# Performance work log

Hardware: AMD Instinct MI355X
Metric: run time of the kernel (lower is better)

Reference implementation:

```python
import jax, jax.numpy as jnp
import numpy as np

B, N, E, H = 4, 2048, 1024, 16
D = E // H  # head dim = 64


def setup_inputs() -> dict:
    key = jax.random.key(0)
    k1, k2, k3 = jax.random.split(key, 3)
    x = jax.random.normal(k1, (B, N, E), dtype=jnp.float32)
    # torch nn.Linear weights are [out_features, in_features]
    w_qkv = jax.random.normal(k2, (3 * E, E), dtype=jnp.float32) * (E ** -0.5)
    w_out = jax.random.normal(k3, (E, E), dtype=jnp.float32) * (E ** -0.5)
    return {"x": x, "w_qkv": w_qkv, "w_out": w_out}


def reference(x, w_qkv, w_out):
    # fused QKV projection: [B,N,E] @ [E,3E] -> [B,N,3E]
    qkv = jnp.einsum("bne,fe->bnf", x, w_qkv)
    q, k, v = jnp.split(qkv, 3, axis=-1)
    # b n (h d) -> b h n d
    split_heads = lambda t: t.reshape(B, N, H, D).transpose(0, 2, 1, 3)
    q, k, v = map(split_heads, (q, k, v))
    scale = D ** -0.5
    scores = jnp.einsum("bhnd,bhmd->bhnm", q, k) * scale
    attn = jax.nn.softmax(scores, axis=-1)
    out = jnp.einsum("bhnm,bhmd->bhnd", attn, v)
    # b h n d -> b n (h d)
    out = out.transpose(0, 2, 1, 3).reshape(B, N, E)
    return jnp.einsum("bne,fe->bnf", out, w_out)
```

## Files before the change

kernel.cpp:

```cpp
#include <hip/hip_runtime.h>
#include <hip/hip_bf16.h>

typedef short bf16x8 __attribute__((ext_vector_type(8)));
typedef float f32x4 __attribute__((ext_vector_type(4)));
using bf16 = __hip_bfloat16;

#define MFMA16(a, b, c) __builtin_amdgcn_mfma_f32_16x16x32_bf16(a, b, c, 0, 0, 0)

typedef unsigned int u32;
typedef u32 __attribute__((address_space(1))) global_u32;
typedef u32 __attribute__((address_space(3))) lds_u32;

__device__ __forceinline__ void gload_lds16(const unsigned short* g, unsigned short* l) {
    __builtin_amdgcn_global_load_lds((const global_u32*)g, (lds_u32*)l, 16, 0, 0);
}

__device__ __forceinline__ short f2b(float f) {
    __hip_bfloat16 h = __float2bfloat16(f);
    return *reinterpret_cast<short*>(&h);
}

__global__ __launch_bounds__(256) void cvt3_kernel(const float* __restrict__ x,
                                                   const float* __restrict__ wq,
                                                   const float* __restrict__ wo,
                                                   unsigned short* __restrict__ xb,
                                                   unsigned short* __restrict__ wqb,
                                                   unsigned short* __restrict__ wob) {
    const int id = blockIdx.x;
    const float* src;
    unsigned short* dst;
    size_t off;
    if (id < 4096) {
        src = x; dst = xb; off = (size_t)id * 2048;
    } else if (id < 5632) {
        src = wq; dst = wqb; off = (size_t)(id - 4096) * 2048;
    } else {
        src = wo; dst = wob; off = (size_t)(id - 5632) * 2048;
    }
    const size_t i = off + (size_t)threadIdx.x * 8;
    float4 v0 = *(const float4*)(src + i);
    float4 v1 = *(const float4*)(src + i + 4);
    bf16x8 o;
    o[0] = f2b(v0.x); o[1] = f2b(v0.y); o[2] = f2b(v0.z); o[3] = f2b(v0.w);
    o[4] = f2b(v1.x); o[5] = f2b(v1.y); o[6] = f2b(v1.z); o[7] = f2b(v1.w);
    *(bf16x8*)(dst + i) = o;
}

template <int MODE>
__global__ __launch_bounds__(256) void gemm128_kernel(const unsigned short* __restrict__ A,
                                                      const unsigned short* __restrict__ W,
                                                      void* __restrict__ outp) {
    __shared__ unsigned short As[128][64];
    __shared__ unsigned short Ws[128][64];
    const int tid = threadIdx.x;
    const int lane = tid & 63;
    const int w = tid >> 6;
    const int wr = w >> 1, wc = w & 1;
    const int lm = lane & 15, quad = lane >> 4;
    const int m0 = blockIdx.y * 128, n0 = blockIdx.x * 128;

    const int srow8 = lane >> 3;
    const int skg = (lane & 7) ^ srow8;
    const unsigned short* Ag = A + (size_t)(m0 + w * 32 + srow8) * 1024 + skg * 8;
    const unsigned short* Wg = W + (size_t)(n0 + w * 32 + srow8) * 1024 + skg * 8;

    f32x4 acc[4][4] = {};

    for (int k0 = 0; k0 < 1024; k0 += 64) {
        __syncthreads();
#pragma unroll
        for (int j = 0; j < 4; j++) {
            gload_lds16(Ag + j * (8 * 1024), &As[w * 32 + j * 8][0]);
            gload_lds16(Wg + j * (8 * 1024), &Ws[w * 32 + j * 8][0]);
        }
        Ag += 64;
        Wg += 64;
        __syncthreads();
#pragma unroll
        for (int ks = 0; ks < 2; ks++) {
            const int swz = ((quad + ks * 4) ^ (lm & 7)) * 8;
            bf16x8 af[4], bf[4];
#pragma unroll
            for (int mt = 0; mt < 4; mt++)
                af[mt] = *(const bf16x8*)&As[wr * 64 + mt * 16 + lm][swz];
#pragma unroll
            for (int nt = 0; nt < 4; nt++)
                bf[nt] = *(const bf16x8*)&Ws[wc * 64 + nt * 16 + lm][swz];
#pragma unroll
            for (int mt = 0; mt < 4; mt++)
#pragma unroll
                for (int nt = 0; nt < 4; nt++)
                    acc[mt][nt] = MFMA16(af[mt], bf[nt], acc[mt][nt]);
        }
    }

#pragma unroll
    for (int mt = 0; mt < 4; mt++)
#pragma unroll
        for (int nt = 0; nt < 4; nt++) {
            f32x4 v = acc[mt][nt];
            const int gr0 = m0 + wr * 64 + mt * 16 + quad * 4;
            const int gc = n0 + wc * 64 + nt * 16 + lm;
            if (MODE == 2) {
                bf16* qkv = (bf16*)outp;
                const int which = gc >> 10;
                const int h = (gc >> 6) & 15;
                const int d = gc & 63;
                const int b = gr0 >> 11, n = gr0 & 2047;
                if (which == 2) {
                    short4 pk;
                    pk.x = f2b(v[0]); pk.y = f2b(v[1]); pk.z = f2b(v[2]); pk.w = f2b(v[3]);
                    *(short4*)&qkv[2ull * 8388608 +
                                   ((size_t)((b * 16 + h) * 64 + d)) * 2048 + n] = pk;
                } else {
#pragma unroll
                    for (int r = 0; r < 4; r++) {
                        float val = v[r];
                        if (which == 0) val *= 0.125f;
                        qkv[(size_t)which * 8388608 +
                            ((size_t)((b * 16 + h) * 2048 + n + r)) * 64 + d] =
                            __float2bfloat16(val);
                    }
                }
            } else {
                float* o = (float*)outp;
#pragma unroll
                for (int r = 0; r < 4; r++) o[(size_t)(gr0 + r) * 1024 + gc] = v[r];
            }
        }
}

__global__ __launch_bounds__(256, 4) void attn_mfma_kernel(
    const unsigned short* __restrict__ Qg, const unsigned short* __restrict__ Kg,
    const unsigned short* __restrict__ Vtg, unsigned short* __restrict__ O) {
    __shared__ unsigned short Ks[64][64];
    __shared__ unsigned short Vs[64][64];
    __shared__ unsigned short Ps[4][2][16][64];
    const int tid = threadIdx.x;
    const int lane = tid & 63;
    const int w = tid >> 6;
    const int lm = lane & 15;
    const int quad = lane >> 4;
    const int bh = blockIdx.x & 63;
    const int n0 = (blockIdx.x >> 6) * 128;
    const size_t base = (size_t)bh * (2048 * 64);

    bf16x8 qf[2][2];
#pragma unroll
    for (int mt = 0; mt < 2; mt++)
#pragma unroll
        for (int ks = 0; ks < 2; ks++)
            qf[mt][ks] = *(const bf16x8*)&Qg[base +
                                            (size_t)(n0 + w * 32 + mt * 16 + lm) * 64 +
                                            ks * 32 + quad * 8];

    f32x4 accO[2][4] = {};
    float lst[2] = {0.f, 0.f};

    const int sr = lane >> 3;
    const int sg = (lane & 7) ^ sr;

    for (int t = 0; t < 32; t++) {
        const int k0 = t * 64;
        __syncthreads();
#pragma unroll
        for (int j = 0; j < 2; j++) {
            const int row = w * 16 + j * 8 + sr;
            gload_lds16(&Kg[base + (size_t)(k0 + row) * 64 + sg * 8], &Ks[w * 16 + j * 8][0]);
            gload_lds16(&Vtg[base + (size_t)row * 2048 + k0 + sg * 8], &Vs[w * 16 + j * 8][0]);
        }
        __syncthreads();

        bf16x8 kb[4][2];
#pragma unroll
        for (int kt = 0; kt < 4; kt++)
#pragma unroll
            for (int ks = 0; ks < 2; ks++)
                kb[kt][ks] = *(const bf16x8*)&Ks[kt * 16 + lm]
                                               [(((ks * 4 + quad) ^ (lm & 7)) * 8)];
        f32x4 s[2][4];
#pragma unroll
        for (int mt = 0; mt < 2; mt++)
#pragma unroll
            for (int kt = 0; kt < 4; kt++) {
                f32x4 z = {};
                z = MFMA16(kb[kt][0], qf[mt][0], z);
                s[mt][kt] = MFMA16(kb[kt][1], qf[mt][1], z);
            }

#pragma unroll
        for (int mt = 0; mt < 2; mt++) {
            float ps = 0.f;
#pragma unroll
            for (int kt = 0; kt < 4; kt++) {
                const float p0 = __expf(s[mt][kt][0]);
                const float p1 = __expf(s[mt][kt][1]);
                const float p2 = __expf(s[mt][kt][2]);
                const float p3 = __expf(s[mt][kt][3]);
                ps += (p0 + p1) + (p2 + p3);
                short4 pk;
                pk.x = f2b(p0); pk.y = f2b(p1); pk.z = f2b(p2); pk.w = f2b(p3);
                const int g = kt * 2 + (quad >> 1);
                *(short4*)&Ps[w][mt][lm][((g ^ (lm & 7)) * 8) + (quad & 1) * 4] = pk;
            }
            lst[mt] += ps;
        }

        bf16x8 vbf[4][2];
#pragma unroll
        for (int nt = 0; nt < 4; nt++)
#pragma unroll
            for (int ks = 0; ks < 2; ks++)
                vbf[nt][ks] = *(const bf16x8*)&Vs[nt * 16 + lm]
                                                [(((ks * 4 + quad) ^ (lm & 7)) * 8)];
#pragma unroll
        for (int mt = 0; mt < 2; mt++) {
            bf16x8 pb0 = *(const bf16x8*)&Ps[w][mt][lm][(((quad) ^ (lm & 7)) * 8)];
            bf16x8 pb1 = *(const bf16x8*)&Ps[w][mt][lm][(((4 + quad) ^ (lm & 7)) * 8)];
#pragma unroll
            for (int nt = 0; nt < 4; nt++) {
                f32x4 a = MFMA16(vbf[nt][0], pb0, accO[mt][nt]);
                accO[mt][nt] = MFMA16(vbf[nt][1], pb1, a);
            }
        }
    }

#pragma unroll
    for (int mt = 0; mt < 2; mt++) {
        lst[mt] += __shfl_xor(lst[mt], 16);
        lst[mt] += __shfl_xor(lst[mt], 32);
    }

    const int b = bh >> 4, h = bh & 15;
#pragma unroll
    for (int mt = 0; mt < 2; mt++) {
        const float inv = 1.0f / lst[mt];
        const int n = n0 + w * 32 + mt * 16 + lm;
#pragma unroll
        for (int nt = 0; nt < 4; nt++) {
            short4 pk;
            pk.x = f2b(accO[mt][nt][0] * inv);
            pk.y = f2b(accO[mt][nt][1] * inv);
            pk.z = f2b(accO[mt][nt][2] * inv);
            pk.w = f2b(accO[mt][nt][3] * inv);
            *(short4*)&O[((size_t)(b * 2048 + n)) * 1024 + h * 64 + nt * 16 + quad * 4] = pk;
        }
    }
}

extern "C" void kernel_launch(void* const* d_in, const int* in_sizes, int n_in,
                              void* d_out, int out_size, void* d_ws, size_t ws_size,
                              hipStream_t stream) {
    const float* x = (const float*)d_in[0];
    const float* w_qkv = (const float*)d_in[1];
    const float* w_out = (const float*)d_in[2];
    float* out = (float*)d_out;

    unsigned short* qkvb = (unsigned short*)d_ws;
    unsigned short* xb = qkvb + 3ull * 8388608;
    unsigned short* wqkvb = xb + 8388608;
    unsigned short* woutb = wqkvb + 3145728;

    cvt3_kernel<<<6144, 256, 0, stream>>>(x, w_qkv, w_out, xb, wqkvb, woutb);
    gemm128_kernel<2><<<dim3(24, 64), 256, 0, stream>>>(xb, wqkvb, (void*)qkvb);
    attn_mfma_kernel<<<1024, 256, 0, stream>>>(qkvb, qkvb + 8388608,
                                               qkvb + 2 * 8388608, xb);
    gemm128_kernel<1><<<dim3(8, 64), 256, 0, stream>>>(xb, woutb, out);
}
```

Measured before the change: 261.9 us.

## Replace QKV projection GEMM with 256x256-tile double-buffered 8-wave kernel

Adds a new QKV projection kernel that computes 256x256 output tiles with 512 threads. It double-buffers A and B tiles in LDS through direct global-to-LDS loads, interleaving loads with MFMA phases and raising wave priority during the math. It also remaps block IDs so neighbouring blocks share tiles in cache. The larger tile increases data reuse per byte loaded, but uses more LDS and registers, which lowers occupancy. Only 384 blocks are launched, which may leave some CUs underused.

```diff
diff --git a/kernel.cpp b/kernel.cpp
--- a/kernel.cpp
+++ b/kernel.cpp
@@ -130,6 +130,155 @@
         }
 }
 
+__global__ __launch_bounds__(512, 2) void gemm256_qkv_kernel(
+    const unsigned short* __restrict__ A,
+    const unsigned short* __restrict__ W,
+    unsigned short* __restrict__ qkvp) {
+    __shared__ unsigned short As[2][256][64];
+    __shared__ unsigned short Bs[2][256][64];
+    const int tid = threadIdx.x;
+    const int lane = tid & 63;
+    const int w = tid >> 6;
+    const int wr = w >> 2, wc = w & 3;
+    const int lm = lane & 15, quad = lane >> 4;
+
+    const int id = blockIdx.x;
+    const int xs = (id & 7) * 48 + (id >> 3);
+    const int n0 = (xs % 12) * 256;
+    const int m0 = (xs / 12) * 256;
+
+    const int sr = lane >> 3;
+    const int sg = (lane & 7) ^ sr;
+    const unsigned short* Ab = A + (size_t)(m0 + w * 8 + sr) * 1024 + sg * 8;
+    const unsigned short* Wb = W + (size_t)(n0 + w * 8 + sr) * 1024 + sg * 8;
+
+    f32x4 acc[8][4] = {};
+    bf16x8 af[4][2];
+    bf16x8 bfr[4][2];
+
+#define STAGE_A(buf, half, kk)                                                     \
+    do {                                                                           \
+        gload_lds16(Ab + (size_t)((half) * 128) * 1024 + (kk),                     \
+                    &As[buf][(half) * 128 + w * 8][0]);                            \
+        gload_lds16(Ab + (size_t)((half) * 128 + 64) * 1024 + (kk),                \
+                    &As[buf][(half) * 128 + 64 + w * 8][0]);                       \
+    } while (0)
+#define STAGE_B(buf, half, kk)                                                     \
+    do {                                                                           \
+        gload_lds16(Wb + (size_t)((half) * 128) * 1024 + (kk),                     \
+                    &Bs[buf][(half) * 128 + w * 8][0]);                            \
+        gload_lds16(Wb + (size_t)((half) * 128 + 64) * 1024 + (kk),                \
+                    &Bs[buf][(half) * 128 + 64 + w * 8][0]);                       \
+    } while (0)
+#define LDA(buf, mh)                                                               \
+    do {                                                                           \
+        _Pragma("unroll") for (int mt2 = 0; mt2 < 4; mt2++)                        \
+            _Pragma("unroll") for (int ks = 0; ks < 2; ks++)                       \
+                af[mt2][ks] = *(const bf16x8*)&As[buf][wr * 128 + (mh) * 64 +      \
+                                                       mt2 * 16 + lm]              \
+                                                 [(((quad + ks * 4) ^ (lm & 7)) *  \
+                                                   8)];                            \
+    } while (0)
+#define LDB(buf, nh)                                                               \
+    do {                                                                           \
+        _Pragma("unroll") for (int nt2 = 0; nt2 < 2; nt2++)                        \
+            _Pragma("unroll") for (int ks = 0; ks < 2; ks++)                       \
+                bfr[(nh) * 2 + nt2][ks] =                                          \
+                    *(const bf16x8*)&Bs[buf][wc * 64 + ((nh) * 2 + nt2) * 16 + lm] \
+                                        [(((quad + ks * 4) ^ (lm & 7)) * 8)];      \
+    } while (0)
+#define PHASE_MM(mh, nh)                                                           \
+    do {                                                                           \
+        __builtin_amdgcn_s_barrier();                                              \
+        asm volatile("s_waitcnt lgkmcnt(0)" ::: "memory");                         \
+        __builtin_amdgcn_s_setprio(1);                                             \
+        _Pragma("unroll") for (int mt2 = 0; mt2 < 4; mt2++)                        \
+            _Pragma("unroll") for (int nt2 = 0; nt2 < 2; nt2++) {                  \
+                f32x4 t0 = MFMA16(af[mt2][0], bfr[(nh) * 2 + nt2][0],              \
+                                  acc[(mh) * 4 + mt2][(nh) * 2 + nt2]);            \
+                acc[(mh) * 4 + mt2][(nh) * 2 + nt2] =                              \
+                    MFMA16(af[mt2][1], bfr[(nh) * 2 + nt2][1], t0);                \
+            }                                                                      \
+        __builtin_amdgcn_s_setprio(0);                                             \
+        __builtin_amdgcn_s_barrier();                                              \
+    } while (0)
+#define VMCNT4 asm volatile("s_waitcnt vmcnt(4)" ::: "memory")
+
+    STAGE_A(0, 0, 0); STAGE_A(0, 1, 0);
+    STAGE_B(0, 0, 0); STAGE_B(0, 1, 0);
+    STAGE_B(1, 0, 64); STAGE_B(1, 1, 64);
+    VMCNT4;
+    __builtin_amdgcn_s_barrier();
+
+    for (int i = 0; i < 8; i++) {
+        const int t = 2 * i;
+        const int k1 = (t + 1) * 64;
+        const int k2 = (t + 2 < 16) ? (t + 2) * 64 : 0;
+        const int k3 = (t + 3 < 16) ? (t + 3) * 64 : 0;
+        LDA(0, 0); LDB(0, 0);
+        STAGE_A(1, 0, k1);
+        PHASE_MM(0, 0);
+        LDB(0, 1);
+        STAGE_A(1, 1, k1);
+        PHASE_MM(0, 1);
+        LDA(0, 1);
+        STAGE_B(0, 0, k2);
+        PHASE_MM(1, 1);
+        STAGE_B(0, 1, k2);
+        VMCNT4;
+        PHASE_MM(1, 0);
+        LDA(1, 0); LDB(1, 0);
+        STAGE_A(0, 0, k2);
+        PHASE_MM(0, 0);
+        LDB(1, 1);
+        STAGE_A(0, 1, k2);
+        PHASE_MM(0, 1);
+        LDA(1, 1);
+        STAGE_B(1, 0, k3);
+        PHASE_MM(1, 1);
+        STAGE_B(1, 1, k3);
+        VMCNT4;
+        PHASE_MM(1, 0);
+    }
+
+    asm volatile("s_waitcnt vmcnt(0)" ::: "memory");
+
+    bf16* qkv = (bf16*)qkvp;
+#pragma unroll
+    for (int mt = 0; mt < 8; mt++)
+#pragma unroll
+        for (int nt = 0; nt < 4; nt++) {
+            f32x4 v = acc[mt][nt];
+            const int gr0 = m0 + wr * 128 + mt * 16 + quad * 4;
+            const int gc = n0 + wc * 64 + nt * 16 + lm;
+            const int which = gc >> 10;
+            const int h = (gc >> 6) & 15;
+            const int d = gc & 63;
+            const int b = gr0 >> 11, n = gr0 & 2047;
+            if (which == 2) {
+                short4 pk;
+                pk.x = f2b(v[0]); pk.y = f2b(v[1]); pk.z = f2b(v[2]); pk.w = f2b(v[3]);
+                *(short4*)&qkv[2ull * 8388608 +
+                               ((size_t)((b * 16 + h) * 64 + d)) * 2048 + n] = pk;
+            } else {
+#pragma unroll
+                for (int r = 0; r < 4; r++) {
+                    float val = v[r];
+                    if (which == 0) val *= 0.125f;
+                    qkv[(size_t)which * 8388608 +
+                        ((size_t)((b * 16 + h) * 2048 + n + r)) * 64 + d] =
+                        __float2bfloat16(val);
+                }
+            }
+        }
+#undef STAGE_A
+#undef STAGE_B
+#undef LDA
+#undef LDB
+#undef PHASE_MM
+#undef VMCNT4
+}
+
 __global__ __launch_bounds__(256, 4) void attn_mfma_kernel(
     const unsigned short* __restrict__ Qg, const unsigned short* __restrict__ Kg,
     const unsigned short* __restrict__ Vtg, unsigned short* __restrict__ O) {
@@ -262,7 +411,7 @@
     unsigned short* woutb = wqkvb + 3145728;
 
     cvt3_kernel<<<6144, 256, 0, stream>>>(x, w_qkv, w_out, xb, wqkvb, woutb);
-    gemm128_kernel<2><<<dim3(24, 64), 256, 0, stream>>>(xb, wqkvb, (void*)qkvb);
+    gemm256_qkv_kernel<<<384, 512, 0, stream>>>(xb, wqkvb, qkvb);
     attn_mfma_kernel<<<1024, 256, 0, stream>>>(qkvb, qkvb + 8388608,
                                                qkvb + 2 * 8388608, xb);
     gemm128_kernel<1><<<dim3(8, 64), 256, 0, stream>>>(xb, woutb, out);
```

Measured after the change: 277.6 us. 6.0% more time.
